# Optimization experiments

Measured on AMD Instinct MI355X. Metric: run time of the kernel, lower is better.

Reference implementation:

```python
import jax, jax.numpy as jnp
import numpy as np

H, V, B, T = 1024, 512, 128, 512


def setup_inputs() -> dict:
    key = jax.random.key(0)
    ks = jax.random.split(key, 12)
    return {
        "batch_X": jax.random.normal(ks[0], (B, T, V), jnp.float32),
        "batch_Y": jax.random.randint(ks[1], (B, T), 0, V),
        "Wf": jax.random.normal(ks[2], (H, V + H), jnp.float32) * 0.01,
        "bf": jnp.ones((H, 1), jnp.float32),
        "Wu": jax.random.normal(ks[3], (H, V + H), jnp.float32) * 0.01,
        "bu": jnp.zeros((H, 1), jnp.float32),
        "Wcc": jax.random.normal(ks[4], (H, V + H), jnp.float32) * 0.01,
        "bcc": jnp.zeros((H, 1), jnp.float32),
        "Wo": jax.random.normal(ks[5], (H, V + H), jnp.float32) * 0.01,
        "bo": jnp.zeros((H, 1), jnp.float32),
        "Wy": jax.random.normal(ks[6], (V, H), jnp.float32) * 0.01,
        "by": jnp.zeros((V, 1), jnp.float32),
        "a_prev": jax.random.normal(ks[7], (H, B), jnp.float32),
        "c_prev": jax.random.normal(ks[8], (H, B), jnp.float32),
    }


def reference(batch_X, batch_Y, Wf, bf, Wu, bu, Wcc, bcc, Wo, bo, Wy, by, a_prev, c_prev):
    # (B,T,V) -> (T,V,B), time-major column-vector layout as in the torch code
    x_seq = jnp.transpose(batch_X, (1, 2, 0))
    h = Wf.shape[0]
    # fuse the 4 gate matmuls into one GEMM per step (same math)
    Wg = jnp.concatenate([Wf, Wu, Wcc, Wo], axis=0)       # (4H, H+V)
    bg = jnp.concatenate([bf, bu, bcc, bo], axis=0)       # (4H, 1)

    def step(carry, x_t):
        a, c = carry
        concat = jnp.concatenate([a, x_t], axis=0)        # (H+V, B)
        g = Wg @ concat + bg                              # (4H, B)
        f = jax.nn.sigmoid(g[:h])
        u = jax.nn.sigmoid(g[h:2 * h])
        cc = jnp.tanh(g[2 * h:3 * h])
        o = jax.nn.sigmoid(g[3 * h:])
        c_new = f * c + u * cc
        a_new = o * jnp.tanh(c_new)
        y = Wy @ a_new + by                               # (V, B)
        return (a_new, c_new), y

    (_, _), logits = jax.lax.scan(step, (a_prev, c_prev), x_seq)  # (T, V, B)
    v = Wy.shape[0]
    logits2 = jnp.transpose(logits, (2, 0, 1)).reshape(-1, v)     # (B*T, V)
    logp = jax.nn.log_softmax(logits2, axis=-1)
    labels = batch_Y.reshape(-1)
    loss = -jnp.mean(jnp.take_along_axis(logp, labels[:, None], axis=1))
    return logits2, loss
```

## Files before the change

kernel.cpp:

```cpp
#include <hip/hip_runtime.h>

#define Hh 1024
#define Vv 512
#define Bb 128
#define Tt 512
#define TV (Tt * Vv)

typedef unsigned short u16;
typedef unsigned int u32;
typedef unsigned long long u64;
typedef __attribute__((ext_vector_type(8))) short bf16x8;
typedef __attribute__((ext_vector_type(4))) float floatx4;

#define WS_WGA 0
#define WS_WYA 12582912
#define WS_AF0 13631488
#define WS_AF1 13893632
#define WS_CTRL 14155776

__device__ __forceinline__ u16 f2bf(float f) {
    union { float f; u32 u; } c; c.f = f;
    u32 u = c.u + 0x7fffu + ((c.u >> 16) & 1u);
    return (u16)(u >> 16);
}
__device__ __forceinline__ float sigm(float x) { return 1.0f / (1.0f + __expf(-x)); }
__device__ __forceinline__ float tanh_f(float x) {
    float e = __expf(-2.0f * fabsf(x));
    float t = (1.0f - e) / (1.0f + e);
    return x >= 0.0f ? t : -t;
}
__device__ __forceinline__ bf16x8 load_cohere(const u16* p) {
    union { u64 q[2]; bf16x8 v; } u;
    u64* q = (u64*)p;
    u.q[0] = __hip_atomic_load(q, __ATOMIC_RELAXED, __HIP_MEMORY_SCOPE_AGENT);
    u.q[1] = __hip_atomic_load(q + 1, __ATOMIC_RELAXED, __HIP_MEMORY_SCOPE_AGENT);
    return u.v;
}

__global__ __launch_bounds__(256) void pack_gates(const float* __restrict__ Wf, const float* __restrict__ Wu,
                                                  const float* __restrict__ Wc, const float* __restrict__ Wo,
                                                  u16* __restrict__ WgA) {
    int tid = blockIdx.x * 256 + threadIdx.x;
    int l = tid & 63;
    int q = tid >> 6;
    int g = q & 3; q >>= 2;
    int kt = q % 48; int hc = q / 48;
    const float* W = (g == 0) ? Wf : (g == 1) ? Wu : (g == 2) ? Wc : Wo;
    int row = hc * 16 + (l & 15);
    int k = kt * 32 + (l >> 4) * 8;
    const float* src = W + (size_t)row * 1536 + k;
    float4 a = *(const float4*)src;
    float4 b = *(const float4*)(src + 4);
    bf16x8 v;
    v[0] = (short)f2bf(a.x); v[1] = (short)f2bf(a.y); v[2] = (short)f2bf(a.z); v[3] = (short)f2bf(a.w);
    v[4] = (short)f2bf(b.x); v[5] = (short)f2bf(b.y); v[6] = (short)f2bf(b.z); v[7] = (short)f2bf(b.w);
    *(bf16x8*)(WgA + (size_t)tid * 8) = v;
}

__global__ __launch_bounds__(256) void pack_wy(const float* __restrict__ Wy, u16* __restrict__ WyA) {
    int tid = blockIdx.x * 256 + threadIdx.x;
    int l = tid & 63;
    int q = tid >> 6;
    int kt = q & 31; int i = q >> 5;
    int row = i * 16 + (l & 15);
    int k = kt * 32 + ((l >> 4) & 3) * 8;
    const float* src = Wy + (size_t)row * 1024 + k;
    float4 a = *(const float4*)src;
    float4 b = *(const float4*)(src + 4);
    bf16x8 v;
    v[0] = (short)f2bf(a.x); v[1] = (short)f2bf(a.y); v[2] = (short)f2bf(a.z); v[3] = (short)f2bf(a.w);
    v[4] = (short)f2bf(b.x); v[5] = (short)f2bf(b.y); v[6] = (short)f2bf(b.z); v[7] = (short)f2bf(b.w);
    *(bf16x8*)(WyA + (size_t)tid * 8) = v;
}

__global__ __launch_bounds__(256) void pack_a(const float* __restrict__ ap, u16* __restrict__ aF0) {
    int o = blockIdx.x * 256 + threadIdx.x;
    int j = o & 7, li = (o >> 3) & 63, seg = o >> 9;
    int kt = seg >> 3, ch = seg & 7;
    int h = kt * 32 + ((li >> 4) & 3) * 8 + j;
    int b = ch * 16 + (li & 15);
    aF0[o] = f2bf(ap[(size_t)h * Bb + b]);
}

__global__ __launch_bounds__(512, 2) void lstm_main(
    const float* __restrict__ X, const float* __restrict__ bfp, const float* __restrict__ bup,
    const float* __restrict__ bcp, const float* __restrict__ bop, const float* __restrict__ byp,
    const float* __restrict__ c_prev, const u16* __restrict__ WgA, const u16* __restrict__ WyA,
    u16* __restrict__ aF0, u16* __restrict__ aF1, float* __restrict__ out, u32* __restrict__ flags)
{
    __shared__ __align__(16) u16 xs[32768];
    __shared__ __align__(16) float predG[16384];
    __shared__ __align__(16) float predY[2304];

    const int tid = threadIdx.x;
    const int bid = blockIdx.x;
    const int l = tid & 63;
    const int w = tid >> 6;
    const int hc = bid & 63;
    const int cc2 = bid >> 6;
    const int c0 = cc2 * 32;
    const int fm = l & 15;
    const int fq = l >> 4;
    const int fk = fq * 8;
    u32* gFlags = flags + cc2 * 64;

    const int em = tid >> 5;
    const int en = tid & 31;
    const int hrow = hc * 16 + em;
    const int bcol = c0 + en;
    float c_val = c_prev[(size_t)hrow * Bb + bcol];
    const float bfv = bfp[hrow], buv = bup[hrow], bcv = bcp[hrow], bov = bop[hrow];
    const int a_kt = hrow >> 5;
    const int a_q = (hrow >> 3) & 3;
    const int a_j = hrow & 7;
    const int a_ch = bcol >> 4;
    const int a_lane = (a_q << 4) | (bcol & 15);
    const int aWidx = ((a_kt << 3) + a_ch) * 512 + a_lane * 8 + a_j;
    const int rcol = (en + ((em & 12) << 1)) & 31;
    const int yi = hc >> 1;
    const int ych = hc & 1;
    const int ybch = (cc2 << 1) | ych;

    floatx4 acc[4][2];
    auto zacc = [&]() {
#pragma unroll
        for (int g = 0; g < 4; ++g)
#pragma unroll
            for (int c = 0; c < 2; ++c) acc[g][c] = (floatx4){0.f, 0.f, 0.f, 0.f};
    };
    auto xpart = [&](int tt) {
        const u16* xbuf = xs + (tt & 1) * 16384;
#pragma unroll
        for (int kk = 0; kk < 2; ++kk) {
            int ktx = (w << 1) + kk;
            const u16* bp = xbuf + (size_t)(ktx << 1) * 512 + (l << 3);
            bf16x8 b0 = *(const bf16x8*)bp;
            bf16x8 b1 = *(const bf16x8*)(bp + 512);
            const u16* ap = WgA + (size_t)((hc * 48 + 32 + ktx) << 2) * 512 + (l << 3);
#pragma unroll
            for (int g = 0; g < 4; ++g) {
                bf16x8 a = *(const bf16x8*)(ap + (size_t)g * 512);
                acc[g][0] = __builtin_amdgcn_mfma_f32_16x16x32_bf16(a, b0, acc[g][0], 0, 0, 0);
                acc[g][1] = __builtin_amdgcn_mfma_f32_16x16x32_bf16(a, b1, acc[g][1], 0, 0, 0);
            }
        }
    };
    auto stage_direct = [&](int tt) {
        const float* Xt = X + (size_t)tt * Vv;
        u16* xdst = xs + (tt & 1) * 16384;
#pragma unroll
        for (int it = 0; it < 4; ++it) {
            int s = w + (it << 3);
            int kt2 = s >> 1, half = s & 1;
            int b = c0 + (half << 4) + fm;
            const float* p = Xt + (size_t)b * TV + kt2 * 32 + fk;
            float4 a = *(const float4*)p;
            float4 bx = *(const float4*)(p + 4);
            bf16x8 v;
            v[0] = (short)f2bf(a.x); v[1] = (short)f2bf(a.y); v[2] = (short)f2bf(a.z); v[3] = (short)f2bf(a.w);
            v[4] = (short)f2bf(bx.x); v[5] = (short)f2bf(bx.y); v[6] = (short)f2bf(bx.z); v[7] = (short)f2bf(bx.w);
            *(bf16x8*)(xdst + s * 512 + (l << 3)) = v;
        }
    };
    auto barrier_wait = [&](u32 gen) {
        if (tid < 64) {
            while (1) {
                u32 v = __hip_atomic_load(gFlags + l, __ATOMIC_RELAXED, __HIP_MEMORY_SCOPE_AGENT);
                if (__all(v >= gen)) break;
                __builtin_amdgcn_s_sleep(2);
            }
        }
        __builtin_amdgcn_fence(__ATOMIC_ACQUIRE, "workgroup");
        __syncthreads();
    };

    stage_direct(0);
    stage_direct(1);
    __syncthreads();
    zacc();
    xpart(0);

    for (int t = 0; t < Tt; ++t) {
        if (t > 0) barrier_wait((u32)t);
        const u16* aCur = (t & 1) ? aF1 : aF0;
        u16* aNxt = (t & 1) ? aF0 : aF1;

        floatx4 yacc = {0.f, 0.f, 0.f, 0.f};
#pragma unroll
        for (int kk = 0; kk < 4; ++kk) {
            const int kt = (w << 2) + kk;
            const u16* bp = aCur + (size_t)((kt << 3) + (cc2 << 1)) * 512 + (l << 3);
            bf16x8 b0 = load_cohere(bp);
            bf16x8 b1 = load_cohere(bp + 512);
            const u16* ap = WgA + (size_t)((hc * 48 + kt) << 2) * 512 + (l << 3);
#pragma unroll
            for (int g = 0; g < 4; ++g) {
                bf16x8 a = *(const bf16x8*)(ap + (size_t)g * 512);
                acc[g][0] = __builtin_amdgcn_mfma_f32_16x16x32_bf16(a, b0, acc[g][0], 0, 0, 0);
                acc[g][1] = __builtin_amdgcn_mfma_f32_16x16x32_bf16(a, b1, acc[g][1], 0, 0, 0);
            }
            if (t > 0) {
                bf16x8 ya = *(const bf16x8*)(WyA + (size_t)(yi * 32 + kt) * 512 + (l << 3));
                if (ych) yacc = __builtin_amdgcn_mfma_f32_16x16x32_bf16(ya, b1, yacc, 0, 0, 0);
                else     yacc = __builtin_amdgcn_mfma_f32_16x16x32_bf16(ya, b0, yacc, 0, 0, 0);
            }
        }

        {
            float* pw = predG + w * 2048;
#pragma unroll
            for (int g = 0; g < 4; ++g)
#pragma unroll
                for (int c = 0; c < 2; ++c)
#pragma unroll
                    for (int r = 0; r < 4; ++r)
                        pw[((g << 4) + (fq << 2) + r) * 32 + (((c << 4) + fm + (fq << 3)) & 31)] = acc[g][c][r];
            if (t > 0) {
                float* py = predY + w * 272;
#pragma unroll
                for (int r = 0; r < 4; ++r) py[((fq << 2) + r) * 17 + fm] = yacc[r];
            }
        }
        __syncthreads();

        {
            float s0 = 0.f, s1 = 0.f, s2 = 0.f, s3 = 0.f;
#pragma unroll
            for (int ks = 0; ks < 8; ++ks) {
                const float* pk = predG + ks * 2048 + em * 32 + rcol;
                s0 += pk[0]; s1 += pk[512]; s2 += pk[1024]; s3 += pk[1536];
            }
            float f = sigm(s0 + bfv), u = sigm(s1 + buv);
            float ccv = tanh_f(s2 + bcv), oo = sigm(s3 + bov);
            c_val = f * c_val + u * ccv;
            float a_new = oo * tanh_f(c_val);
            u32 me = (u32)f2bf(a_new);
            u32 other = (u32)__shfl_xor((int)me, 32);
            if (l < 32) {
                u32 packed = me | (other << 16);
                __hip_atomic_store((u32*)aNxt + (aWidx >> 1), packed, __ATOMIC_RELAXED, __HIP_MEMORY_SCOPE_AGENT);
            }
            if (t > 0 && tid < 256) {
                int n = tid >> 4, m = tid & 15;
                float s = 0.f;
#pragma unroll
                for (int ww = 0; ww < 8; ++ww) s += predY[ww * 272 + m * 17 + n];
                s += byp[(yi << 4) + m];
                out[(size_t)((cc2 << 5) + (ych << 4) + n) * TV + (size_t)(t - 1) * Vv + (yi << 4) + m] = s;
            }
        }
        asm volatile("s_waitcnt vmcnt(0)" ::: "memory");
        __syncthreads();

        if (tid == 0)
            __hip_atomic_store(gFlags + hc, (u32)(t + 1), __ATOMIC_RELAXED, __HIP_MEMORY_SCOPE_AGENT);

        float4 xr[4][2];
        const bool doStage = (t + 2 < Tt);
        if (doStage) {
            const float* Xt = X + (size_t)(t + 2) * Vv;
#pragma unroll
            for (int it = 0; it < 4; ++it) {
                int s = w + (it << 3);
                int kt2 = s >> 1, half = s & 1;
                int b = c0 + (half << 4) + fm;
                const float* p = Xt + (size_t)b * TV + kt2 * 32 + fk;
                xr[it][0] = *(const float4*)p;
                xr[it][1] = *(const float4*)(p + 4);
            }
        }
        zacc();
        if (t + 1 < Tt) xpart(t + 1);
        if (doStage) {
            u16* xdst = xs + (t & 1) * 16384;
#pragma unroll
            for (int it = 0; it < 4; ++it) {
                int s = w + (it << 3);
                bf16x8 v;
                v[0] = (short)f2bf(xr[it][0].x); v[1] = (short)f2bf(xr[it][0].y);
                v[2] = (short)f2bf(xr[it][0].z); v[3] = (short)f2bf(xr[it][0].w);
                v[4] = (short)f2bf(xr[it][1].x); v[5] = (short)f2bf(xr[it][1].y);
                v[6] = (short)f2bf(xr[it][1].z); v[7] = (short)f2bf(xr[it][1].w);
                *(bf16x8*)(xdst + s * 512 + (l << 3)) = v;
            }
        }
    }

    barrier_wait((u32)Tt);
    {
        const u16* aCur = (Tt & 1) ? aF1 : aF0;
        floatx4 yacc = {0.f, 0.f, 0.f, 0.f};
#pragma unroll
        for (int kk = 0; kk < 4; ++kk) {
            const int kt = (w << 2) + kk;
            bf16x8 ya = *(const bf16x8*)(WyA + (size_t)(yi * 32 + kt) * 512 + (l << 3));
            bf16x8 b = load_cohere(aCur + (size_t)((kt << 3) + ybch) * 512 + (l << 3));
            yacc = __builtin_amdgcn_mfma_f32_16x16x32_bf16(ya, b, yacc, 0, 0, 0);
        }
        float* py = predY + w * 272;
#pragma unroll
        for (int r = 0; r < 4; ++r) py[((fq << 2) + r) * 17 + fm] = yacc[r];
        __syncthreads();
        if (tid < 256) {
            int n = tid >> 4, m = tid & 15;
            float s = 0.f;
#pragma unroll
            for (int ww = 0; ww < 8; ++ww) s += predY[ww * 272 + m * 17 + n];
            s += byp[(yi << 4) + m];
            out[(size_t)((cc2 << 5) + (ych << 4) + n) * TV + (size_t)(Tt - 1) * Vv + (yi << 4) + m] = s;
        }
    }
}

__global__ __launch_bounds__(256) void loss_k(const float* __restrict__ logits, const int* __restrict__ Y,
                                              float* __restrict__ acc) {
    int w = threadIdx.x >> 6, l = threadIdx.x & 63;
    int rbase = blockIdx.x * 256 + w * 64;
    float sum = 0.f;
    for (int i = 0; i < 64; ++i) {
        const float* row = logits + (size_t)(rbase + i) * Vv;
        float4 v0 = *(const float4*)(row + l * 8);
        float4 v1 = *(const float4*)(row + l * 8 + 4);
        float vals[8] = {v0.x, v0.y, v0.z, v0.w, v1.x, v1.y, v1.z, v1.w};
        float mx = vals[0];
#pragma unroll
        for (int j = 1; j < 8; ++j) mx = fmaxf(mx, vals[j]);
#pragma unroll
        for (int s = 1; s < 64; s <<= 1) mx = fmaxf(mx, __shfl_xor(mx, s, 64));
        float es = 0.f;
#pragma unroll
        for (int j = 0; j < 8; ++j) es += __expf(vals[j] - mx);
#pragma unroll
        for (int s = 1; s < 64; s <<= 1) es += __shfl_xor(es, s, 64);
        int label = Y[rbase + i];
        float xl_local = vals[0];
#pragma unroll
        for (int j = 1; j < 8; ++j) xl_local = ((label & 7) == j) ? vals[j] : xl_local;
        float xl = __shfl(xl_local, label >> 3, 64);
        sum += (mx + __logf(es)) - xl;
    }
    if (l == 0) atomicAdd(acc, sum);
}

__global__ void finalize_k(const float* __restrict__ acc, float* __restrict__ out) {
    if (threadIdx.x == 0) out[(size_t)Bb * Tt * Vv] = acc[0] * (1.0f / (Bb * Tt));
}

extern "C" void kernel_launch(void* const* d_in, const int* in_sizes, int n_in,
                              void* d_out, int out_size, void* d_ws, size_t ws_size,
                              hipStream_t stream) {
    const float* X  = (const float*)d_in[0];
    const int*   Y  = (const int*)d_in[1];
    const float* Wf = (const float*)d_in[2];
    const float* bf = (const float*)d_in[3];
    const float* Wu = (const float*)d_in[4];
    const float* bu = (const float*)d_in[5];
    const float* Wc = (const float*)d_in[6];
    const float* bc = (const float*)d_in[7];
    const float* Wo = (const float*)d_in[8];
    const float* bo = (const float*)d_in[9];
    const float* Wy = (const float*)d_in[10];
    const float* by = (const float*)d_in[11];
    const float* ap = (const float*)d_in[12];
    const float* cp = (const float*)d_in[13];
    float* out = (float*)d_out;
    char* ws = (char*)d_ws;
    u16* WgA = (u16*)(ws + WS_WGA);
    u16* WyA = (u16*)(ws + WS_WYA);
    u16* aF0 = (u16*)(ws + WS_AF0);
    u16* aF1 = (u16*)(ws + WS_AF1);
    u32* flags = (u32*)(ws + WS_CTRL);
    float* lossAcc = (float*)(ws + WS_CTRL + 1024);

    hipMemsetAsync((void*)flags, 0, 2048, stream);
    pack_gates<<<3072, 256, 0, stream>>>(Wf, Wu, Wc, Wo, WgA);
    pack_wy<<<256, 256, 0, stream>>>(Wy, WyA);
    pack_a<<<512, 256, 0, stream>>>(ap, aF0);

    void* args[] = {(void*)&X, (void*)&bf, (void*)&bu, (void*)&bc, (void*)&bo, (void*)&by,
                    (void*)&cp, (void*)&WgA, (void*)&WyA, (void*)&aF0, (void*)&aF1,
                    (void*)&out, (void*)&flags};
    hipLaunchCooperativeKernel((void*)lstm_main, dim3(256), dim3(512), args, 0, stream);

    loss_k<<<256, 256, 0, stream>>>(out, Y, lossAcc);
    finalize_k<<<1, 64, 0, stream>>>(lossAcc, out);
}
```

Baseline: 3.912 ms.

## Replace block-wide flag barrier with per-wave waits and defer Wy projection

Each wave now polls only the eight producer flags covering the k-slices it consumes, which removes the workgroup-wide __syncthreads after the spin-wait so waves can start their gate MFMAs independently. The output-logit MFMA and its reduction and store are moved off the recurrent critical path and run after the flag release, reusing the cached a-fragments. This aims to shorten the serial per-step latency of the recurrence. In exchange it adds an extra __syncthreads per step and keeps more registers live.

Result: faster. 3.633 ms (-7.1%).

```diff
diff --git a/kernel.cpp b/kernel.cpp
--- a/kernel.cpp
+++ b/kernel.cpp
@@ -97,16 +97,16 @@
     const int l = tid & 63;
     const int w = tid >> 6;
     const int hc = bid & 63;
-    const int cc2 = bid >> 6;
+    const int grp = bid >> 6;
+    const int cc2 = grp;
     const int c0 = cc2 * 32;
     const int fm = l & 15;
     const int fq = l >> 4;
-    const int fk = fq * 8;
     u32* gFlags = flags + cc2 * 64;
 
     const int em = tid >> 5;
     const int en = tid & 31;
-    const int hrow = hc * 16 + em;
+    const int hrow = (hc << 4) + em;
     const int bcol = c0 + en;
     float c_val = c_prev[(size_t)hrow * Bb + bcol];
     const float bfv = bfp[hrow], buv = bup[hrow], bcv = bcp[hrow], bov = bop[hrow];
@@ -153,7 +153,7 @@
             int s = w + (it << 3);
             int kt2 = s >> 1, half = s & 1;
             int b = c0 + (half << 4) + fm;
-            const float* p = Xt + (size_t)b * TV + kt2 * 32 + fk;
+            const float* p = Xt + (size_t)b * TV + kt2 * 32 + (fq << 3);
             float4 a = *(const float4*)p;
             float4 bx = *(const float4*)(p + 4);
             bf16x8 v;
@@ -162,16 +162,14 @@
             *(bf16x8*)(xdst + s * 512 + (l << 3)) = v;
         }
     };
-    auto barrier_wait = [&](u32 gen) {
-        if (tid < 64) {
-            while (1) {
-                u32 v = __hip_atomic_load(gFlags + l, __ATOMIC_RELAXED, __HIP_MEMORY_SCOPE_AGENT);
-                if (__all(v >= gen)) break;
-                __builtin_amdgcn_s_sleep(2);
-            }
+    auto wave_wait = [&](u32 gen) {
+        const u32 src = (u32)((w << 3) + (l & 7));
+        while (1) {
+            u32 v = __hip_atomic_load(gFlags + src, __ATOMIC_RELAXED, __HIP_MEMORY_SCOPE_AGENT);
+            if (__all(v >= gen)) break;
+            __builtin_amdgcn_s_sleep(2);
         }
         __builtin_amdgcn_fence(__ATOMIC_ACQUIRE, "workgroup");
-        __syncthreads();
     };
 
     stage_direct(0);
@@ -181,17 +179,18 @@
     xpart(0);
 
     for (int t = 0; t < Tt; ++t) {
-        if (t > 0) barrier_wait((u32)t);
         const u16* aCur = (t & 1) ? aF1 : aF0;
         u16* aNxt = (t & 1) ? aF0 : aF1;
-
-        floatx4 yacc = {0.f, 0.f, 0.f, 0.f};
+        if (t > 0) wave_wait((u32)t);
+
+        bf16x8 bsel[4];
 #pragma unroll
         for (int kk = 0; kk < 4; ++kk) {
             const int kt = (w << 2) + kk;
             const u16* bp = aCur + (size_t)((kt << 3) + (cc2 << 1)) * 512 + (l << 3);
             bf16x8 b0 = load_cohere(bp);
             bf16x8 b1 = load_cohere(bp + 512);
+            bsel[kk] = ych ? b1 : b0;
             const u16* ap = WgA + (size_t)((hc * 48 + kt) << 2) * 512 + (l << 3);
 #pragma unroll
             for (int g = 0; g < 4; ++g) {
@@ -199,11 +198,6 @@
                 acc[g][0] = __builtin_amdgcn_mfma_f32_16x16x32_bf16(a, b0, acc[g][0], 0, 0, 0);
                 acc[g][1] = __builtin_amdgcn_mfma_f32_16x16x32_bf16(a, b1, acc[g][1], 0, 0, 0);
             }
-            if (t > 0) {
-                bf16x8 ya = *(const bf16x8*)(WyA + (size_t)(yi * 32 + kt) * 512 + (l << 3));
-                if (ych) yacc = __builtin_amdgcn_mfma_f32_16x16x32_bf16(ya, b1, yacc, 0, 0, 0);
-                else     yacc = __builtin_amdgcn_mfma_f32_16x16x32_bf16(ya, b0, yacc, 0, 0, 0);
-            }
         }
 
         {
@@ -215,11 +209,6 @@
 #pragma unroll
                     for (int r = 0; r < 4; ++r)
                         pw[((g << 4) + (fq << 2) + r) * 32 + (((c << 4) + fm + (fq << 3)) & 31)] = acc[g][c][r];
-            if (t > 0) {
-                float* py = predY + w * 272;
-#pragma unroll
-                for (int r = 0; r < 4; ++r) py[((fq << 2) + r) * 17 + fm] = yacc[r];
-            }
         }
         __syncthreads();
 
@@ -236,22 +225,12 @@
             float a_new = oo * tanh_f(c_val);
             u32 me = (u32)f2bf(a_new);
             u32 other = (u32)__shfl_xor((int)me, 32);
-            if (l < 32) {
-                u32 packed = me | (other << 16);
-                __hip_atomic_store((u32*)aNxt + (aWidx >> 1), packed, __ATOMIC_RELAXED, __HIP_MEMORY_SCOPE_AGENT);
-            }
-            if (t > 0 && tid < 256) {
-                int n = tid >> 4, m = tid & 15;
-                float s = 0.f;
-#pragma unroll
-                for (int ww = 0; ww < 8; ++ww) s += predY[ww * 272 + m * 17 + n];
-                s += byp[(yi << 4) + m];
-                out[(size_t)((cc2 << 5) + (ych << 4) + n) * TV + (size_t)(t - 1) * Vv + (yi << 4) + m] = s;
-            }
+            if (l < 32)
+                __hip_atomic_store((u32*)aNxt + (aWidx >> 1), me | (other << 16),
+                                   __ATOMIC_RELAXED, __HIP_MEMORY_SCOPE_AGENT);
         }
         asm volatile("s_waitcnt vmcnt(0)" ::: "memory");
         __syncthreads();
-
         if (tid == 0)
             __hip_atomic_store(gFlags + hc, (u32)(t + 1), __ATOMIC_RELAXED, __HIP_MEMORY_SCOPE_AGENT);
 
@@ -264,10 +243,22 @@
                 int s = w + (it << 3);
                 int kt2 = s >> 1, half = s & 1;
                 int b = c0 + (half << 4) + fm;
-                const float* p = Xt + (size_t)b * TV + kt2 * 32 + fk;
+                const float* p = Xt + (size_t)b * TV + kt2 * 32 + (fq << 3);
                 xr[it][0] = *(const float4*)p;
                 xr[it][1] = *(const float4*)(p + 4);
             }
+        }
+        if (t > 0) {
+            floatx4 yacc = {0.f, 0.f, 0.f, 0.f};
+#pragma unroll
+            for (int kk = 0; kk < 4; ++kk) {
+                const int kt = (w << 2) + kk;
+                bf16x8 ya = *(const bf16x8*)(WyA + (size_t)(yi * 32 + kt) * 512 + (l << 3));
+                yacc = __builtin_amdgcn_mfma_f32_16x16x32_bf16(ya, bsel[kk], yacc, 0, 0, 0);
+            }
+            float* py = predY + w * 272;
+#pragma unroll
+            for (int r = 0; r < 4; ++r) py[((fq << 2) + r) * 17 + fm] = yacc[r];
         }
         zacc();
         if (t + 1 < Tt) xpart(t + 1);
@@ -284,18 +275,28 @@
                 *(bf16x8*)(xdst + s * 512 + (l << 3)) = v;
             }
         }
+        __syncthreads();
+        if (t > 0 && tid < 256) {
+            int n = tid >> 4, m = tid & 15;
+            float s = 0.f;
+#pragma unroll
+            for (int ww = 0; ww < 8; ++ww) s += predY[ww * 272 + m * 17 + n];
+            s += byp[(yi << 4) + m];
+            out[(size_t)((cc2 << 5) + (ych << 4) + n) * TV + (size_t)(t - 1) * Vv + (yi << 4) + m] = s;
+        }
     }
 
-    barrier_wait((u32)Tt);
+    wave_wait((u32)Tt);
+    __syncthreads();
     {
         const u16* aCur = (Tt & 1) ? aF1 : aF0;
         floatx4 yacc = {0.f, 0.f, 0.f, 0.f};
 #pragma unroll
         for (int kk = 0; kk < 4; ++kk) {
             const int kt = (w << 2) + kk;
+            bf16x8 b0 = load_cohere(aCur + (size_t)((kt << 3) + ybch) * 512 + (l << 3));
             bf16x8 ya = *(const bf16x8*)(WyA + (size_t)(yi * 32 + kt) * 512 + (l << 3));
-            bf16x8 b = load_cohere(aCur + (size_t)((kt << 3) + ybch) * 512 + (l << 3));
-            yacc = __builtin_amdgcn_mfma_f32_16x16x32_bf16(ya, b, yacc, 0, 0, 0);
+            yacc = __builtin_amdgcn_mfma_f32_16x16x32_bf16(ya, b0, yacc, 0, 0, 0);
         }
         float* py = predY + w * 272;
 #pragma unroll
```
